# Kernel tuning notes

Measured on AMD Instinct MI355X. Metric: run time of the kernel, lower is better.

The kernel has to match this reference:

```python
import jax, jax.numpy as jnp
import numpy as np

N = 100000      # nodes
E = 1600000     # edges (avg degree 16)
F_IN = 64       # num_features
HID = 16        # hidden channels (fixed in module)
OUT = 32        # num_classes
K = 2           # kernel_size (dim=1, degree=1 open B-spline -> 2 basis fns)


def setup_inputs() -> dict:
    key = jax.random.key(0)
    ks = jax.random.split(key, 8)
    return {
        "x": jax.random.normal(ks[0], (N, F_IN), jnp.float32),
        "edge_index": jax.random.randint(ks[1], (2, E), 0, N, dtype=jnp.int64),
        "dropout": 0,  # unused in eval mode (F.dropout training=False)
        "edge_attr": jnp.full((E, 1), 0.1, jnp.float32),  # nt([0.1]) broadcast per edge
        "W1": jax.random.normal(ks[2], (K, F_IN, HID), jnp.float32) / np.sqrt(K * F_IN).astype(np.float32),
        "root1": jax.random.normal(ks[3], (F_IN, HID), jnp.float32) / np.sqrt(F_IN).astype(np.float32),
        "bias1": jnp.zeros((HID,), jnp.float32),
        "W2": jax.random.normal(ks[4], (K, HID, OUT), jnp.float32) / np.sqrt(K * HID).astype(np.float32),
        "root2": jax.random.normal(ks[5], (HID, OUT), jnp.float32) / np.sqrt(HID).astype(np.float32),
        "bias2": jnp.zeros((OUT,), jnp.float32),
    }


def spline_conv(x, edge_index, edge_attr, W, root, bias):
    """SplineConv, dim=1, kernel_size=2, degree=1 open B-spline, aggr='mean'."""
    src, dst = edge_index[0], edge_index[1]
    n = x.shape[0]
    u = edge_attr[:, 0]                                  # [E] pseudo-coords in [0,1]
    # degree-1 open spline, kernel_size=2: frac = u*(ks-1) = u; kernels {0,1}
    basis = jnp.stack([1.0 - u, u], axis=1)              # [E, K]
    # transform at node level (cheaper than gathering raw features per edge)
    h = jnp.einsum('nf,kfo->nko', x, W)                  # [N, K, out]
    msg = jnp.einsum('ek,eko->eo', basis, h[src])        # [E, out]
    summed = jax.ops.segment_sum(msg, dst, num_segments=n)
    deg = jax.ops.segment_sum(jnp.ones_like(u), dst, num_segments=n)
    out = summed / jnp.maximum(deg, 1.0)[:, None]        # mean aggregation
    return out + x @ root + bias                          # root weight + bias


def reference(x, edge_index, dropout, edge_attr, W1, root1, bias1, W2, root2, bias2):
    # dropout is a no-op in eval mode
    h = jax.nn.elu(spline_conv(x, edge_index, edge_attr, W1, root1, bias1))
    h = spline_conv(h, edge_index, edge_attr, W2, root2, bias2)
    return jax.nn.log_softmax(h, axis=1)
```

## Files before the change

### kernel.cpp

```cpp
#include <hip/hip_runtime.h>
#include <math.h>

#define NN 100000
#define NE 1600000
#define F_IN 64
#define HID 16
#define OUTF 32
#define BKT_SHIFT 6
#define BKT_NODES 64
#define NBKT 1563
#define SRCM 0x1FFFF
#define CAP_REG 2048
#define CAP_LDS 1536
#define PBLK2 500
#define EPB2 3200
#define OVF_MAX 4096

__device__ __forceinline__ unsigned bf16r(float f) {
    unsigned u = __float_as_uint(f);
    return (u + 0x7FFFu + ((u >> 16) & 1u)) >> 16;
}
__device__ __forceinline__ float bfa(unsigned p) { return __uint_as_float(p << 16); }
__device__ __forceinline__ float bfd(unsigned p) { return __uint_as_float(p & 0xFFFF0000u); }
__device__ __forceinline__ float bfh(unsigned short v) { return __uint_as_float(((unsigned)v) << 16); }

__device__ __forceinline__ void acc8(uint4 hv, float u, float* s0, float* s1) {
    unsigned w[4] = {hv.x, hv.y, hv.z, hv.w};
#pragma unroll
    for (int q = 0; q < 4; ++q) {
        float lo = __uint_as_float(w[q] << 16);
        float hi = __uint_as_float(w[q] & 0xFFFF0000u);
        s0[2 * q]     += lo; s1[2 * q]     = fmaf(u, lo, s1[2 * q]);
        s0[2 * q + 1] += hi; s1[2 * q + 1] = fmaf(u, hi, s1[2 * q + 1]);
    }
}
__device__ __forceinline__ void acc4(uint4 ap, float u, float* a) {
    unsigned w[4] = {ap.x, ap.y, ap.z, ap.w};
#pragma unroll
    for (int q = 0; q < 4; ++q)
        a[q] += fmaf(u, bfd(w[q]), bfa(w[q]));
}

__global__ __launch_bounds__(256) void zeroG_kernel(int* __restrict__ gcur,
                                                    int* __restrict__ novf) {
    int t = blockIdx.x * 256 + threadIdx.x;
    if (t < NBKT) gcur[t] = 0;
    if (t == NBKT) novf[0] = 0;
}

__global__ __launch_bounds__(1024) void partF_kernel(const int* __restrict__ ei,
                                                     const float* __restrict__ ea,
                                                     int* __restrict__ gcur,
                                                     int* __restrict__ novf,
                                                     int4* __restrict__ ovf,
                                                     int2* __restrict__ bkt) {
    __shared__ int hcnt[NBKT];
    __shared__ int hbase[NBKT];
    __shared__ int lbase[NBKT];
    __shared__ int s[1024];
    __shared__ int2 sbuf[EPB2];
    __shared__ unsigned short bid[EPB2];
    int t = threadIdx.x, blk = blockIdx.x;
    for (int i = t; i < NBKT; i += 1024) hcnt[i] = 0;
    __syncthreads();
    int beg = blk * EPB2;
    int4 d4 = make_int4(0, 0, 0, 0);
    bool act = (4 * t) < EPB2;
    if (act) {
        d4 = *(const int4*)(ei + NE + beg + 4 * t);
        atomicAdd(&hcnt[d4.x >> BKT_SHIFT], 1);
        atomicAdd(&hcnt[d4.y >> BKT_SHIFT], 1);
        atomicAdd(&hcnt[d4.z >> BKT_SHIFT], 1);
        atomicAdd(&hcnt[d4.w >> BKT_SHIFT], 1);
    }
    __syncthreads();
    int i0 = 2 * t, i1 = 2 * t + 1;
    int v0 = (i0 < NBKT) ? hcnt[i0] : 0;
    int v1 = (i1 < NBKT) ? hcnt[i1] : 0;
    s[t] = v0 + v1;
    __syncthreads();
    for (int off = 1; off < 1024; off <<= 1) {
        int xv = (t >= off) ? s[t - off] : 0;
        __syncthreads();
        s[t] += xv;
        __syncthreads();
    }
    int run = (t == 0) ? 0 : s[t - 1];
    if (i0 < NBKT) lbase[i0] = run;
    if (i1 < NBKT) lbase[i1] = run + v0;
    __syncthreads();
    for (int i = t; i < NBKT; i += 1024) {
        int c = hcnt[i];
        hbase[i] = c ? atomicAdd(&gcur[i], c) : 0;
        hcnt[i] = 0;
    }
    __syncthreads();
    if (act) {
        int4 s4 = *(const int4*)(ei + beg + 4 * t);
        float4 u4 = *(const float4*)(ea + beg + 4 * t);
        int dst[4] = {d4.x, d4.y, d4.z, d4.w};
        int src[4] = {s4.x, s4.y, s4.z, s4.w};
        float uu[4] = {u4.x, u4.y, u4.z, u4.w};
#pragma unroll
        for (int k = 0; k < 4; ++k) {
            int b = dst[k] >> BKT_SHIFT;
            int r = atomicAdd(&hcnt[b], 1);
            int lp = lbase[b] + r;
            sbuf[lp] = make_int2(src[k] | ((dst[k] & (BKT_NODES - 1)) << 17),
                                 __float_as_int(uu[k]));
            bid[lp] = (unsigned short)b;
        }
    }
    __syncthreads();
    for (int i = t; i < EPB2; i += 1024) {
        int2 pk = sbuf[i];
        int b = bid[i];
        int p = hbase[b] + (i - lbase[b]);
        if (p < CAP_REG) {
            bkt[(size_t)b * CAP_REG + p] = pk;
        } else {
            int o = atomicAdd(novf, 1);
            if (o < OVF_MAX)
                ovf[o] = make_int4(b * BKT_NODES + (((unsigned)pk.x) >> 17), pk.x & SRCM, pk.y, 0);
        }
    }
}

__global__ __launch_bounds__(256) void proj1_kernel(const float* __restrict__ x,
                                                    const float* __restrict__ W1,
                                                    const float* __restrict__ root1,
                                                    const float* __restrict__ bias1,
                                                    unsigned* __restrict__ ab1p,
                                                    float* __restrict__ r1) {
    __shared__ float w[2 * F_IN * HID];
    __shared__ float wr[F_IN * HID];
    __shared__ float bb[HID];
    for (int i = threadIdx.x; i < 2 * F_IN * HID; i += 256) w[i] = W1[i];
    for (int i = threadIdx.x; i < F_IN * HID; i += 256) wr[i] = root1[i];
    if (threadIdx.x < HID) bb[threadIdx.x] = bias1[threadIdx.x];
    __syncthreads();
    int n = blockIdx.x * 256 + threadIdx.x;
    if (n >= NN) return;
    float accA[HID], accB[HID], accR[HID];
#pragma unroll
    for (int o = 0; o < HID; ++o) { accA[o] = 0.f; accB[o] = 0.f; accR[o] = bb[o]; }
    const float4* xr4 = (const float4*)(x + (size_t)n * F_IN);
    for (int f4 = 0; f4 < F_IN / 4; ++f4) {
        float4 xv4 = xr4[f4];
        float xs[4] = {xv4.x, xv4.y, xv4.z, xv4.w};
#pragma unroll
        for (int q = 0; q < 4; ++q) {
            int f = f4 * 4 + q;
            float xv = xs[q];
            const float* w0 = &w[f * HID];
            const float* w1 = &w[F_IN * HID + f * HID];
            const float* w2 = &wr[f * HID];
#pragma unroll
            for (int o = 0; o < HID; ++o) {
                accA[o] = fmaf(xv, w0[o], accA[o]);
                accB[o] = fmaf(xv, w1[o], accB[o]);
                accR[o] = fmaf(xv, w2[o], accR[o]);
            }
        }
    }
    unsigned* ar = ab1p + (size_t)n * HID;
    float* rr = r1 + (size_t)n * HID;
#pragma unroll
    for (int o = 0; o < HID; ++o) {
        ar[o] = bf16r(accA[o]) | (bf16r(accB[o] - accA[o]) << 16);
        rr[o] = accR[o];
    }
}

__global__ __launch_bounds__(512) void gather1_kernel(const int* __restrict__ gcur,
                                                      const int* __restrict__ novf,
                                                      const int4* __restrict__ ovf,
                                                      int2* __restrict__ bkt,
                                                      const unsigned* __restrict__ ab1p,
                                                      const float* __restrict__ r1,
                                                      unsigned short* __restrict__ h16,
                                                      float* __restrict__ dinv,
                                                      int* __restrict__ segg) {
    __shared__ int2 raw[CAP_LDS];
    __shared__ int2 sorted[CAP_LDS];
    __shared__ int cnt[BKT_NODES], cur[BKT_NODES], segb[BKT_NODES + 1];
    __shared__ float degsL[BKT_NODES];
    int t = threadIdx.x;
    int b = blockIdx.x;
    int tot = gcur[b];
    int beg = b * CAP_REG;
    if (t < BKT_NODES) { cnt[t] = 0; cur[t] = 0; degsL[t] = 0.f; }
    __syncthreads();
    int nodeBase = b * BKT_NODES;

    if (tot <= CAP_LDS) {
        int nv = tot >> 1;
        const int4* g4 = (const int4*)(bkt + beg);
        int4* r4 = (int4*)raw;
        for (int i = t; i < nv; i += 512) r4[i] = g4[i];
        if (t == 0 && (tot & 1)) raw[tot - 1] = bkt[beg + tot - 1];
        __syncthreads();
        for (int e = t; e < tot; e += 512)
            atomicAdd(&cnt[((unsigned)raw[e].x) >> 17], 1);
        __syncthreads();
        if (t < BKT_NODES) {
            int v = cnt[t];
            int sc = v;
#pragma unroll
            for (int off = 1; off < 64; off <<= 1) {
                int o = __shfl_up(sc, off, 64);
                if (t >= off) sc += o;
            }
            segb[t] = sc - v;
            if (t == 63) segb[64] = sc;
        }
        __syncthreads();
        for (int e = t; e < tot; e += 512) {
            int2 pk = raw[e];
            int loc = ((unsigned)pk.x) >> 17;
            int pos = segb[loc] + atomicAdd(&cur[loc], 1);
            sorted[pos] = pk;
        }
        __syncthreads();
        int4* s4 = (int4*)sorted;
        int4* o4 = (int4*)(bkt + beg);
        for (int i = t; i < nv; i += 512) o4[i] = s4[i];
        if (t == 0 && (tot & 1)) bkt[beg + tot - 1] = sorted[tot - 1];
        if (t <= BKT_NODES) segg[b * (BKT_NODES + 1) + t] = segb[t];
        int node = t >> 3;
        int sub = (t >> 2) & 1;
        int jq = t & 3;
        int s0 = segb[node], e2 = segb[node + 1];
        float acc[4] = {0.f, 0.f, 0.f, 0.f};
        int e = s0 + sub;
        for (; e + 6 < e2; e += 8) {
            int2 p0 = sorted[e];
            int2 p1 = sorted[e + 2];
            int2 p2 = sorted[e + 4];
            int2 p3 = sorted[e + 6];
            uint4 a0 = *(const uint4*)(ab1p + ((size_t)(p0.x & SRCM) << 4) + (jq << 2));
            uint4 a1 = *(const uint4*)(ab1p + ((size_t)(p1.x & SRCM) << 4) + (jq << 2));
            uint4 a2 = *(const uint4*)(ab1p + ((size_t)(p2.x & SRCM) << 4) + (jq << 2));
            uint4 a3 = *(const uint4*)(ab1p + ((size_t)(p3.x & SRCM) << 4) + (jq << 2));
            acc4(a0, __int_as_float(p0.y), acc);
            acc4(a1, __int_as_float(p1.y), acc);
            acc4(a2, __int_as_float(p2.y), acc);
            acc4(a3, __int_as_float(p3.y), acc);
        }
        for (; e < e2; e += 2) {
            int2 pk = sorted[e];
            uint4 ap = *(const uint4*)(ab1p + ((size_t)(pk.x & SRCM) << 4) + (jq << 2));
            acc4(ap, __int_as_float(pk.y), acc);
        }
#pragma unroll
        for (int k = 0; k < 4; ++k) acc[k] += __shfl_xor(acc[k], 4);
        if (sub == 0) {
            int n = nodeBase + node;
            if (n < NN) {
                float d0 = 1.f / (float)max(e2 - s0, 1);
                float4 rv = *(const float4*)(r1 + ((size_t)n << 4) + (jq << 2));
                float rr[4] = {rv.x, rv.y, rv.z, rv.w};
                unsigned hw[4];
#pragma unroll
                for (int k = 0; k < 4; ++k) {
                    float v = acc[k] * d0 + rr[k];
                    hw[k] = bf16r(v > 0.f ? v : expm1f(v));
                }
                *(uint2*)(h16 + ((size_t)n << 4) + (jq << 2)) =
                    make_uint2(hw[0] | (hw[1] << 16), hw[2] | (hw[3] << 16));
                if (jq == 0) dinv[n] = d0;
            }
        }
    } else {
        float* accL = (float*)raw;
        int inreg = min(tot, CAP_REG);
        int end = beg + inreg;
        for (int i = t; i < BKT_NODES * HID; i += 512) accL[i] = 0.f;
        __syncthreads();
        int j = t & (HID - 1);
        int g = t >> 4;
        for (int e = beg + g; e < end; e += 32) {
            int2 pk = bkt[e];
            unsigned p = ab1p[(size_t)(pk.x & SRCM) * HID + j];
            atomicAdd(&accL[(((unsigned)pk.x) >> 17) * HID + j],
                      fmaf(__int_as_float(pk.y), bfd(p), bfa(p)));
            if (j == 0) atomicAdd(&degsL[((unsigned)pk.x) >> 17], 1.f);
        }
        int ovn = min(novf[0], OVF_MAX);
        for (int o = 0; o < ovn; ++o) {
            int4 ent = ovf[o];
            int loc = ent.x - nodeBase;
            if (loc >= 0 && loc < BKT_NODES && g == 0) {
                unsigned p = ab1p[(size_t)ent.y * HID + j];
                atomicAdd(&accL[loc * HID + j], fmaf(__int_as_float(ent.z), bfd(p), bfa(p)));
                if (j == 0) atomicAdd(&degsL[loc], 1.f);
            }
        }
        __syncthreads();
        if (t < BKT_NODES) degsL[t] = 1.f / fmaxf(degsL[t], 1.f);
        if (t == 0) segg[b * (BKT_NODES + 1)] = -1;
        __syncthreads();
#pragma unroll
        for (int it = 0; it < BKT_NODES * HID / 512; ++it) {
            int idx = it * 512 + t;
            int nl = idx >> 4, jj = idx & (HID - 1);
            int n = nodeBase + nl;
            if (n < NN) {
                float v = accL[idx] * degsL[nl] + r1[(size_t)n * HID + jj];
                h16[(size_t)n * HID + jj] = (unsigned short)bf16r(v > 0.f ? v : expm1f(v));
            }
        }
        if (t < BKT_NODES && nodeBase + t < NN) dinv[nodeBase + t] = degsL[t];
    }
}

__global__ __launch_bounds__(512) void gather2_kernel(const int* __restrict__ gcur,
                                                      const int* __restrict__ novf,
                                                      const int4* __restrict__ ovf,
                                                      const int2* __restrict__ bkt,
                                                      const unsigned short* __restrict__ h16,
                                                      const float* __restrict__ W2,
                                                      const float* __restrict__ root2,
                                                      const float* __restrict__ bias2,
                                                      const float* __restrict__ dinv,
                                                      const int* __restrict__ segg,
                                                      float* __restrict__ out) {
    __shared__ int segb[BKT_NODES + 1];
    __shared__ float s0L[BKT_NODES * HID];
    __shared__ float s1L[BKT_NODES * HID];
    __shared__ float hloc[BKT_NODES * HID];
    __shared__ float w20[HID * OUTF], w2d[HID * OUTF], wr[HID * OUTF];
    __shared__ float bb[OUTF];
    int t = threadIdx.x;
    for (int i = t; i < HID * OUTF; i += 512) {
        float a = W2[i];
        w20[i] = a;
        w2d[i] = W2[HID * OUTF + i] - a;
        wr[i] = root2[i];
    }
    if (t < OUTF) bb[t] = bias2[t];
    int b = blockIdx.x;
    int tot = gcur[b];
    int beg = b * CAP_REG;
    int nodeBase = b * BKT_NODES;
    if (t <= BKT_NODES) segb[t] = segg[b * (BKT_NODES + 1) + t];
    if (t < BKT_NODES * HID / 8) {
        uint4 hv = ((const uint4*)(h16 + ((size_t)nodeBase << 4)))[t];
        unsigned w4[4] = {hv.x, hv.y, hv.z, hv.w};
#pragma unroll
        for (int q = 0; q < 4; ++q) {
            hloc[t * 8 + 2 * q]     = __uint_as_float(w4[q] << 16);
            hloc[t * 8 + 2 * q + 1] = __uint_as_float(w4[q] & 0xFFFF0000u);
        }
    }
    __syncthreads();

    if (tot <= CAP_LDS && segb[0] != -1) {
        const int2* sp = bkt + beg;
        int node = t >> 3;
        int sub = (t >> 1) & 3;
        int jh = t & 1;
        int s = segb[node], e2 = segb[node + 1];
        float s0[8] = {0.f, 0.f, 0.f, 0.f, 0.f, 0.f, 0.f, 0.f};
        float s1[8] = {0.f, 0.f, 0.f, 0.f, 0.f, 0.f, 0.f, 0.f};
        int e = s + sub;
        for (; e + 12 < e2; e += 16) {
            int2 p0 = sp[e];
            int2 p1 = sp[e + 4];
            int2 p2 = sp[e + 8];
            int2 p3 = sp[e + 12];
            uint4 h0 = *(const uint4*)(h16 + ((size_t)(p0.x & SRCM) << 4) + (jh << 3));
            uint4 h1 = *(const uint4*)(h16 + ((size_t)(p1.x & SRCM) << 4) + (jh << 3));
            uint4 h2 = *(const uint4*)(h16 + ((size_t)(p2.x & SRCM) << 4) + (jh << 3));
            uint4 h3 = *(const uint4*)(h16 + ((size_t)(p3.x & SRCM) << 4) + (jh << 3));
            acc8(h0, __int_as_float(p0.y), s0, s1);
            acc8(h1, __int_as_float(p1.y), s0, s1);
            acc8(h2, __int_as_float(p2.y), s0, s1);
            acc8(h3, __int_as_float(p3.y), s0, s1);
        }
        for (; e < e2; e += 4) {
            int2 pk = sp[e];
            uint4 hv = *(const uint4*)(h16 + ((size_t)(pk.x & SRCM) << 4) + (jh << 3));
            acc8(hv, __int_as_float(pk.y), s0, s1);
        }
#pragma unroll
        for (int k = 0; k < 8; ++k) {
            s0[k] += __shfl_xor(s0[k], 2); s0[k] += __shfl_xor(s0[k], 4);
            s1[k] += __shfl_xor(s1[k], 2); s1[k] += __shfl_xor(s1[k], 4);
        }
        if (sub == 0) {
            int base = node * HID + jh * 8;
#pragma unroll
            for (int k = 0; k < 8; ++k) { s0L[base + k] = s0[k]; s1L[base + k] = s1[k]; }
        }
        __syncthreads();
    } else {
        int inreg = min(tot, CAP_REG);
        int end = beg + inreg;
        for (int i = t; i < BKT_NODES * HID; i += 512) { s0L[i] = 0.f; s1L[i] = 0.f; }
        __syncthreads();
        int j = t & (HID - 1);
        int g = t >> 4;
        for (int e = beg + g; e < end; e += 32) {
            int2 pk = bkt[e];
            float hvv = bfh(h16[(size_t)(pk.x & SRCM) * HID + j]);
            int l = ((unsigned)pk.x) >> 17;
            atomicAdd(&s0L[l * HID + j], hvv);
            atomicAdd(&s1L[l * HID + j], __int_as_float(pk.y) * hvv);
        }
        int ovn = min(novf[0], OVF_MAX);
        for (int o = 0; o < ovn; ++o) {
            int4 ent = ovf[o];
            int loc = ent.x - nodeBase;
            if (loc >= 0 && loc < BKT_NODES && g == 0) {
                float hvv = bfh(h16[(size_t)ent.y * HID + j]);
                atomicAdd(&s0L[loc * HID + j], hvv);
                atomicAdd(&s1L[loc * HID + j], __int_as_float(ent.z) * hvv);
            }
        }
        __syncthreads();
    }

#pragma unroll
    for (int it = 0; it < BKT_NODES * OUTF / 512; ++it) {
        int idx = it * 512 + t;
        int nl = idx >> 5, jj = idx & (OUTF - 1);
        int n = nodeBase + nl;
        float v = 0.f;
        if (n < NN) {
            float msum = 0.f;
            const float* S0 = &s0L[nl * HID];
            const float* S1 = &s1L[nl * HID];
#pragma unroll
            for (int f = 0; f < HID; ++f)
                msum += S0[f] * w20[f * OUTF + jj] + S1[f] * w2d[f * OUTF + jj];
            v = msum * dinv[n] + bb[jj];
            const float* hr = &hloc[nl * HID];
#pragma unroll
            for (int f = 0; f < HID; ++f)
                v = fmaf(hr[f], wr[f * OUTF + jj], v);
        }
        float m = v;
#pragma unroll
        for (int mask = 16; mask >= 1; mask >>= 1) m = fmaxf(m, __shfl_xor(m, mask));
        float ex = expf(v - m);
        float sm = ex;
#pragma unroll
        for (int mask = 16; mask >= 1; mask >>= 1) sm += __shfl_xor(sm, mask);
        if (n < NN) out[(size_t)n * OUTF + jj] = v - m - logf(sm);
    }
}

extern "C" void kernel_launch(void* const* d_in, const int* in_sizes, int n_in,
                              void* d_out, int out_size, void* d_ws, size_t ws_size,
                              hipStream_t stream) {
    const float* x     = (const float*)d_in[0];
    const int*   ei    = (const int*)d_in[1];
    const float* ea    = (const float*)d_in[3];
    const float* W1    = (const float*)d_in[4];
    const float* root1 = (const float*)d_in[5];
    const float* bias1 = (const float*)d_in[6];
    const float* W2    = (const float*)d_in[7];
    const float* root2 = (const float*)d_in[8];
    const float* bias2 = (const float*)d_in[9];
    float* out = (float*)d_out;
    float* ws  = (float*)d_ws;

    const size_t N = NN;
    int*            gcur = (int*)(ws);
    int*            novf = (int*)(ws + 2000);
    int4*           ovf  = (int4*)(ws + 2048);
    float*          dinv = ws + 20000;
    int*            segg = (int*)(ws + 120000);
    float*          r1   = ws + 222000;
    unsigned*       ab1p = (unsigned*)(ws + 222000 + 16 * N);
    unsigned short* h16  = (unsigned short*)(ws + 222000 + 32 * N);
    int2*           bkt  = (int2*)(ws + 222000 + 40 * N);

    int nbN = (NN + 255) / 256;
    zeroG_kernel<<<(NBKT + 256) / 256, 256, 0, stream>>>(gcur, novf);
    partF_kernel<<<PBLK2, 1024, 0, stream>>>(ei, ea, gcur, novf, ovf, bkt);
    proj1_kernel<<<nbN, 256, 0, stream>>>(x, W1, root1, bias1, ab1p, r1);
    gather1_kernel<<<NBKT, 512, 0, stream>>>(gcur, novf, ovf, bkt, ab1p, r1, h16, dinv, segg);
    gather2_kernel<<<NBKT, 512, 0, stream>>>(gcur, novf, ovf, bkt, h16, W2, root2, bias2, dinv, segg, out);
}
```

Measured before the change: 124.7 us.

## Shrink gather blocks to 256 threads, split gather2 into half-buckets, drop raw LDS staging

Gather1 now runs 256 threads per block and reads bucket entries straight from global memory for the counting sort, which removes the separate raw LDS staging array and halves its shared-memory footprint. Each node is now handled by 4 threads that walk all of its edges, replacing 8 threads plus a shuffle reduction. Gather2 is split into two 256-thread blocks per bucket, each handling 32 nodes, so twice as many smaller blocks run. The intent is better occupancy and less LDS per block. The cost is reading bucket entries from global memory twice in gather1 and less edge-level parallelism per node.

```diff
diff --git a/kernel.cpp b/kernel.cpp
--- a/kernel.cpp
+++ b/kernel.cpp
@@ -172,7 +172,7 @@
     }
 }
 
-__global__ __launch_bounds__(512) void gather1_kernel(const int* __restrict__ gcur,
+__global__ __launch_bounds__(256) void gather1_kernel(const int* __restrict__ gcur,
                                                       const int* __restrict__ novf,
                                                       const int4* __restrict__ ovf,
                                                       int2* __restrict__ bkt,
@@ -181,7 +181,6 @@
                                                       unsigned short* __restrict__ h16,
                                                       float* __restrict__ dinv,
                                                       int* __restrict__ segg) {
-    __shared__ int2 raw[CAP_LDS];
     __shared__ int2 sorted[CAP_LDS];
     __shared__ int cnt[BKT_NODES], cur[BKT_NODES], segb[BKT_NODES + 1];
     __shared__ float degsL[BKT_NODES];
@@ -194,14 +193,8 @@
     int nodeBase = b * BKT_NODES;
 
     if (tot <= CAP_LDS) {
-        int nv = tot >> 1;
-        const int4* g4 = (const int4*)(bkt + beg);
-        int4* r4 = (int4*)raw;
-        for (int i = t; i < nv; i += 512) r4[i] = g4[i];
-        if (t == 0 && (tot & 1)) raw[tot - 1] = bkt[beg + tot - 1];
-        __syncthreads();
-        for (int e = t; e < tot; e += 512)
-            atomicAdd(&cnt[((unsigned)raw[e].x) >> 17], 1);
+        for (int e = t; e < tot; e += 256)
+            atomicAdd(&cnt[((unsigned)bkt[beg + e].x) >> 17], 1);
         __syncthreads();
         if (t < BKT_NODES) {
             int v = cnt[t];
@@ -215,29 +208,29 @@
             if (t == 63) segb[64] = sc;
         }
         __syncthreads();
-        for (int e = t; e < tot; e += 512) {
-            int2 pk = raw[e];
+        for (int e = t; e < tot; e += 256) {
+            int2 pk = bkt[beg + e];
             int loc = ((unsigned)pk.x) >> 17;
             int pos = segb[loc] + atomicAdd(&cur[loc], 1);
             sorted[pos] = pk;
         }
         __syncthreads();
+        int nv = tot >> 1;
         int4* s4 = (int4*)sorted;
         int4* o4 = (int4*)(bkt + beg);
-        for (int i = t; i < nv; i += 512) o4[i] = s4[i];
+        for (int i = t; i < nv; i += 256) o4[i] = s4[i];
         if (t == 0 && (tot & 1)) bkt[beg + tot - 1] = sorted[tot - 1];
         if (t <= BKT_NODES) segg[b * (BKT_NODES + 1) + t] = segb[t];
-        int node = t >> 3;
-        int sub = (t >> 2) & 1;
+        int node = t >> 2;
         int jq = t & 3;
         int s0 = segb[node], e2 = segb[node + 1];
         float acc[4] = {0.f, 0.f, 0.f, 0.f};
-        int e = s0 + sub;
-        for (; e + 6 < e2; e += 8) {
+        int e = s0;
+        for (; e + 3 < e2; e += 4) {
             int2 p0 = sorted[e];
-            int2 p1 = sorted[e + 2];
-            int2 p2 = sorted[e + 4];
-            int2 p3 = sorted[e + 6];
+            int2 p1 = sorted[e + 1];
+            int2 p2 = sorted[e + 2];
+            int2 p3 = sorted[e + 3];
             uint4 a0 = *(const uint4*)(ab1p + ((size_t)(p0.x & SRCM) << 4) + (jq << 2));
             uint4 a1 = *(const uint4*)(ab1p + ((size_t)(p1.x & SRCM) << 4) + (jq << 2));
             uint4 a2 = *(const uint4*)(ab1p + ((size_t)(p2.x & SRCM) << 4) + (jq << 2));
@@ -247,39 +240,35 @@
             acc4(a2, __int_as_float(p2.y), acc);
             acc4(a3, __int_as_float(p3.y), acc);
         }
-        for (; e < e2; e += 2) {
+        for (; e < e2; ++e) {
             int2 pk = sorted[e];
             uint4 ap = *(const uint4*)(ab1p + ((size_t)(pk.x & SRCM) << 4) + (jq << 2));
             acc4(ap, __int_as_float(pk.y), acc);
         }
-#pragma unroll
-        for (int k = 0; k < 4; ++k) acc[k] += __shfl_xor(acc[k], 4);
-        if (sub == 0) {
-            int n = nodeBase + node;
-            if (n < NN) {
-                float d0 = 1.f / (float)max(e2 - s0, 1);
-                float4 rv = *(const float4*)(r1 + ((size_t)n << 4) + (jq << 2));
-                float rr[4] = {rv.x, rv.y, rv.z, rv.w};
-                unsigned hw[4];
-#pragma unroll
-                for (int k = 0; k < 4; ++k) {
-                    float v = acc[k] * d0 + rr[k];
-                    hw[k] = bf16r(v > 0.f ? v : expm1f(v));
-                }
-                *(uint2*)(h16 + ((size_t)n << 4) + (jq << 2)) =
-                    make_uint2(hw[0] | (hw[1] << 16), hw[2] | (hw[3] << 16));
-                if (jq == 0) dinv[n] = d0;
-            }
+        int n = nodeBase + node;
+        if (n < NN) {
+            float d0 = 1.f / (float)max(e2 - s0, 1);
+            float4 rv = *(const float4*)(r1 + ((size_t)n << 4) + (jq << 2));
+            float rr[4] = {rv.x, rv.y, rv.z, rv.w};
+            unsigned hw[4];
+#pragma unroll
+            for (int k = 0; k < 4; ++k) {
+                float v = acc[k] * d0 + rr[k];
+                hw[k] = bf16r(v > 0.f ? v : expm1f(v));
+            }
+            *(uint2*)(h16 + ((size_t)n << 4) + (jq << 2)) =
+                make_uint2(hw[0] | (hw[1] << 16), hw[2] | (hw[3] << 16));
+            if (jq == 0) dinv[n] = d0;
         }
     } else {
-        float* accL = (float*)raw;
+        float* accL = (float*)sorted;
         int inreg = min(tot, CAP_REG);
         int end = beg + inreg;
-        for (int i = t; i < BKT_NODES * HID; i += 512) accL[i] = 0.f;
+        for (int i = t; i < BKT_NODES * HID; i += 256) accL[i] = 0.f;
         __syncthreads();
         int j = t & (HID - 1);
         int g = t >> 4;
-        for (int e = beg + g; e < end; e += 32) {
+        for (int e = beg + g; e < end; e += 16) {
             int2 pk = bkt[e];
             unsigned p = ab1p[(size_t)(pk.x & SRCM) * HID + j];
             atomicAdd(&accL[(((unsigned)pk.x) >> 17) * HID + j],
@@ -300,9 +289,7 @@
         if (t < BKT_NODES) degsL[t] = 1.f / fmaxf(degsL[t], 1.f);
         if (t == 0) segg[b * (BKT_NODES + 1)] = -1;
         __syncthreads();
-#pragma unroll
-        for (int it = 0; it < BKT_NODES * HID / 512; ++it) {
-            int idx = it * 512 + t;
+        for (int idx = t; idx < BKT_NODES * HID; idx += 256) {
             int nl = idx >> 4, jj = idx & (HID - 1);
             int n = nodeBase + nl;
             if (n < NN) {
@@ -314,7 +301,8 @@
     }
 }
 
-__global__ __launch_bounds__(512) void gather2_kernel(const int* __restrict__ gcur,
+#define HB_NODES 32
+__global__ __launch_bounds__(256) void gather2_kernel(const int* __restrict__ gcur,
                                                       const int* __restrict__ novf,
                                                       const int4* __restrict__ ovf,
                                                       const int2* __restrict__ bkt,
@@ -325,27 +313,31 @@
                                                       const float* __restrict__ dinv,
                                                       const int* __restrict__ segg,
                                                       float* __restrict__ out) {
-    __shared__ int segb[BKT_NODES + 1];
-    __shared__ float s0L[BKT_NODES * HID];
-    __shared__ float s1L[BKT_NODES * HID];
-    __shared__ float hloc[BKT_NODES * HID];
+    __shared__ int segb[HB_NODES + 1];
+    __shared__ int sflag;
+    __shared__ float s0L[HB_NODES * HID];
+    __shared__ float s1L[HB_NODES * HID];
+    __shared__ float hloc[HB_NODES * HID];
     __shared__ float w20[HID * OUTF], w2d[HID * OUTF], wr[HID * OUTF];
     __shared__ float bb[OUTF];
     int t = threadIdx.x;
-    for (int i = t; i < HID * OUTF; i += 512) {
+    int b2 = blockIdx.x;
+    int b = b2 >> 1;
+    int h = b2 & 1;
+    for (int i = t; i < HID * OUTF; i += 256) {
         float a = W2[i];
         w20[i] = a;
         w2d[i] = W2[HID * OUTF + i] - a;
         wr[i] = root2[i];
     }
     if (t < OUTF) bb[t] = bias2[t];
-    int b = blockIdx.x;
     int tot = gcur[b];
     int beg = b * CAP_REG;
-    int nodeBase = b * BKT_NODES;
-    if (t <= BKT_NODES) segb[t] = segg[b * (BKT_NODES + 1) + t];
-    if (t < BKT_NODES * HID / 8) {
-        uint4 hv = ((const uint4*)(h16 + ((size_t)nodeBase << 4)))[t];
+    int nodeBase = b * BKT_NODES + h * HB_NODES;
+    if (t <= HB_NODES) segb[t] = segg[b * (BKT_NODES + 1) + h * HB_NODES + t];
+    if (t == 0) sflag = segg[b * (BKT_NODES + 1)];
+    if (t < HB_NODES * HID / 8) {
+        uint4 hv = *(const uint4*)(h16 + ((size_t)nodeBase << 4) + t * 8);
         unsigned w4[4] = {hv.x, hv.y, hv.z, hv.w};
 #pragma unroll
         for (int q = 0; q < 4; ++q) {
@@ -355,7 +347,7 @@
     }
     __syncthreads();
 
-    if (tot <= CAP_LDS && segb[0] != -1) {
+    if (tot <= CAP_LDS && sflag != -1) {
         const int2* sp = bkt + beg;
         int node = t >> 3;
         int sub = (t >> 1) & 3;
@@ -397,22 +389,24 @@
     } else {
         int inreg = min(tot, CAP_REG);
         int end = beg + inreg;
-        for (int i = t; i < BKT_NODES * HID; i += 512) { s0L[i] = 0.f; s1L[i] = 0.f; }
+        for (int i = t; i < HB_NODES * HID; i += 256) { s0L[i] = 0.f; s1L[i] = 0.f; }
         __syncthreads();
         int j = t & (HID - 1);
         int g = t >> 4;
-        for (int e = beg + g; e < end; e += 32) {
+        for (int e = beg + g; e < end; e += 16) {
             int2 pk = bkt[e];
-            float hvv = bfh(h16[(size_t)(pk.x & SRCM) * HID + j]);
-            int l = ((unsigned)pk.x) >> 17;
-            atomicAdd(&s0L[l * HID + j], hvv);
-            atomicAdd(&s1L[l * HID + j], __int_as_float(pk.y) * hvv);
+            int loc = ((unsigned)pk.x) >> 17;
+            if ((loc >> 5) == h) {
+                float hvv = bfh(h16[(size_t)(pk.x & SRCM) * HID + j]);
+                atomicAdd(&s0L[(loc & 31) * HID + j], hvv);
+                atomicAdd(&s1L[(loc & 31) * HID + j], __int_as_float(pk.y) * hvv);
+            }
         }
         int ovn = min(novf[0], OVF_MAX);
         for (int o = 0; o < ovn; ++o) {
             int4 ent = ovf[o];
             int loc = ent.x - nodeBase;
-            if (loc >= 0 && loc < BKT_NODES && g == 0) {
+            if (loc >= 0 && loc < HB_NODES && g == 0) {
                 float hvv = bfh(h16[(size_t)ent.y * HID + j]);
                 atomicAdd(&s0L[loc * HID + j], hvv);
                 atomicAdd(&s1L[loc * HID + j], __int_as_float(ent.z) * hvv);
@@ -422,8 +416,8 @@
     }
 
 #pragma unroll
-    for (int it = 0; it < BKT_NODES * OUTF / 512; ++it) {
-        int idx = it * 512 + t;
+    for (int it = 0; it < HB_NODES * OUTF / 256; ++it) {
+        int idx = it * 256 + t;
         int nl = idx >> 5, jj = idx & (OUTF - 1);
         int n = nodeBase + nl;
         float v = 0.f;
@@ -481,6 +475,6 @@
     zeroG_kernel<<<(NBKT + 256) / 256, 256, 0, stream>>>(gcur, novf);
     partF_kernel<<<PBLK2, 1024, 0, stream>>>(ei, ea, gcur, novf, ovf, bkt);
     proj1_kernel<<<nbN, 256, 0, stream>>>(x, W1, root1, bias1, ab1p, r1);
-    gather1_kernel<<<NBKT, 512, 0, stream>>>(gcur, novf, ovf, bkt, ab1p, r1, h16, dinv, segg);
-    gather2_kernel<<<NBKT, 512, 0, stream>>>(gcur, novf, ovf, bkt, h16, W2, root2, bias2, dinv, segg, out);
-}
+    gather1_kernel<<<NBKT, 256, 0, stream>>>(gcur, novf, ovf, bkt, ab1p, r1, h16, dinv, segg);
+    gather2_kernel<<<NBKT * 2, 256, 0, stream>>>(gcur, novf, ovf, bkt, h16, W2, root2, bias2, dinv, segg, out);
+}
```

Result: faster. 120.0 us (-3.7%).
